# Performance work log

Measured on AMD Instinct MI355X. Metric: run time of the kernel, lower is better.

The kernel has to match this reference:

```python
import jax, jax.numpy as jnp
import numpy as np

N, E, E2 = 50000, 100000, 100000
NODE_IN, H, EDGE_IN, EDGE_H = 64, 32, 16, 128
STEPS = 3
ALPHA = 0.5
BETA = 1.0 / STEPS  # forward overwrites self.beta with 1/num_steps
EPS = 1e-5


def setup_inputs() -> dict:
    key = jax.random.key(0)
    ks = jax.random.split(key, 16)
    p = lambda k, shape, s=0.05: (jax.random.normal(k, shape, jnp.float32) * s)
    return {
        "n_feat": jax.random.normal(ks[0], (N, NODE_IN), jnp.float32),
        "e_feat": jax.random.normal(ks[1], (E, EDGE_IN), jnp.float32),
        "src": jax.random.randint(ks[2], (E,), 0, N, jnp.int32),
        "dst": jax.random.randint(ks[3], (E,), 0, N, jnp.int32),
        "src_list": jax.random.randint(ks[4], (E2,), 0, N, jnp.int32),
        "dst_list": jax.random.randint(ks[5], (E2,), 0, N, jnp.int32),
        "lin0_w": p(ks[6], (H, NODE_IN)), "lin0_b": jnp.zeros((H,), jnp.float32),
        "en1_w": p(ks[7], (EDGE_H, EDGE_IN)), "en1_b": jnp.zeros((EDGE_H,), jnp.float32),
        "en2_w": p(ks[8], (H * H, EDGE_H)), "en2_b": jnp.zeros((H * H,), jnp.float32),
        "conv_bias": jnp.zeros((H,), jnp.float32),
        "lin1_w": p(ks[9], (H, H)), "lin1_b": jnp.zeros((H,), jnp.float32),
        "bn_gamma": jnp.ones((H,), jnp.float32), "bn_beta": jnp.zeros((H,), jnp.float32),
        "ylin_w": p(ks[10], (3, H)), "ylin_b": jnp.zeros((3,), jnp.float32),
        "ylin2_w": p(ks[11], (1, H)), "ylin2_b": jnp.zeros((1,), jnp.float32),
    }


def reference(n_feat, e_feat, src, dst, src_list, dst_list,
              lin0_w, lin0_b, en1_w, en1_b, en2_w, en2_b, conv_bias,
              lin1_w, lin1_b, bn_gamma, bn_beta, ylin_w, ylin_b, ylin2_w, ylin2_b):
    n = n_feat.shape[0]
    out = jax.nn.relu(n_feat @ lin0_w.T + lin0_b)
    h0 = out
    # Edge-conditioned weights (eval mode: dropouts are identity, so the
    # edge MLP output is identical every step -> compute once).
    We = (jax.nn.relu(e_feat @ en1_w.T + en1_b) @ en2_w.T + en2_b).reshape(-1, H, H)  # (E,H,H)
    for _ in range(STEPS):
        msg = jnp.einsum('eh,eho->eo', out[src], We)                 # per-edge matvec
        agg = jax.ops.segment_sum(msg, dst, num_segments=n)          # sum aggregator
        conv = agg + out + conv_bias                                 # identity residual + bias
        temp = ALPHA * conv + (1.0 - ALPHA) * h0
        out = jax.nn.relu(BETA * (temp @ lin1_w.T + lin1_b) + (1.0 - BETA) * temp)
    # BatchNorm1d with batch statistics (training-mode stats, biased var)
    mu = out.mean(axis=0)
    var = ((out - mu) ** 2).mean(axis=0)
    y_bn = (out - mu) / jnp.sqrt(var + EPS) * bn_gamma + bn_beta
    y_sigmoid = jax.nn.sigmoid(y_bn @ ylin_w.T + ylin_b)                              # (N,3)
    edge_hop_out = jax.nn.sigmoid((y_bn[src_list] * y_bn[dst_list]) @ ylin2_w.T + ylin2_b)  # (E2,1)
    return (y_sigmoid, edge_hop_out)
```

## Files before the change

kernel.cpp:

```cpp
#include <hip/hip_runtime.h>
#include <hip/hip_bf16.h>
#include <math.h>

#define HH 32
#define NODE_IN 64
#define EDGE_IN 16
#define EDGE_H 128
#define M_TILE 256

typedef __attribute__((ext_vector_type(8))) short bf16x8;
typedef __attribute__((ext_vector_type(4))) float f32x4;

__device__ inline unsigned short f2bf(float f) {
    union { float f; unsigned int u; } v; v.f = f;
    unsigned int r = v.u + 0x7fff + ((v.u >> 16) & 1);
    return (unsigned short)(r >> 16);
}

__device__ inline void gload_lds16(const void* g, void* lds) {
    __builtin_amdgcn_global_load_lds(
        (const __attribute__((address_space(1))) void*)g,
        (__attribute__((address_space(3))) void*)lds, 16, 0, 0);
}

__global__ void k_prep_w2(const float* __restrict__ en2_w, unsigned short* __restrict__ W2s) {
    int i = blockIdx.x * 256 + threadIdx.x;
    int r = i >> 7, q = i & 127;
    int p = q >> 3, sub = q & 7;
    int c = p ^ (r & 15);
    W2s[i] = f2bf(en2_w[r * EDGE_H + c * 8 + sub]);
}

__global__ void __launch_bounds__(256, 4)
k_prep_r(const float* __restrict__ e_feat, const float* __restrict__ en1_w,
         const float* __restrict__ en1_b, unsigned short* __restrict__ Rb,
         int E, int E_pad) {
    int t = threadIdx.x, wave = t >> 6, l = t & 63;
    int lo = l & 15, lq = l >> 4;
    int ebase = blockIdx.x * 256 + wave * 64;

    bf16x8 bfrag[8];
    #pragma unroll
    for (int nt = 0; nt < 8; ++nt) {
        unsigned short br[8] = {0, 0, 0, 0, 0, 0, 0, 0};
        if (lq < 2) {
            const float* wr = en1_w + (nt * 16 + lo) * EDGE_IN + lq * 8;
            #pragma unroll
            for (int z = 0; z < 8; ++z) br[z] = f2bf(wr[z]);
        }
        bfrag[nt] = *(const bf16x8*)br;
    }
    float b1v[8];
    #pragma unroll
    for (int nt = 0; nt < 8; ++nt) b1v[nt] = en1_b[nt * 16 + lo];

    #pragma unroll
    for (int m = 0; m < 4; ++m) {
        int ea = ebase + m * 16 + lo;
        unsigned short ar[8] = {0, 0, 0, 0, 0, 0, 0, 0};
        if (lq < 2 && ea < E) {
            const float* er = e_feat + (size_t)ea * EDGE_IN + lq * 8;
            float4 v0 = ((const float4*)er)[0];
            float4 v1 = ((const float4*)er)[1];
            ar[0] = f2bf(v0.x); ar[1] = f2bf(v0.y); ar[2] = f2bf(v0.z); ar[3] = f2bf(v0.w);
            ar[4] = f2bf(v1.x); ar[5] = f2bf(v1.y); ar[6] = f2bf(v1.z); ar[7] = f2bf(v1.w);
        }
        bf16x8 af = *(const bf16x8*)ar;

        int erow = ebase + m * 16 + lq * 4;
        #pragma unroll
        for (int nt = 0; nt < 8; ++nt) {
            f32x4 acc = (f32x4){b1v[nt], b1v[nt], b1v[nt], b1v[nt]};
            acc = __builtin_amdgcn_mfma_f32_16x16x32_bf16(af, bfrag[nt], acc, 0, 0, 0);
            #pragma unroll
            for (int r = 0; r < 4; ++r)
                Rb[(size_t)(erow + r) * EDGE_H + nt * 16 + lo] = f2bf(fmaxf(acc[r], 0.f));
        }
    }
}

__global__ void k_lin0(const float* __restrict__ nf, const float* __restrict__ w,
                       const float* __restrict__ b, float* __restrict__ out,
                       float* __restrict__ h0, int n) {
    __shared__ float nf_s[8][NODE_IN];
    __shared__ float w_s[HH][NODE_IN + 1];
    int t = threadIdx.x;
    for (int i = t; i < HH * NODE_IN; i += 256) w_s[i / NODE_IN][i % NODE_IN] = w[i];
    int n0 = blockIdx.x * 8;
    for (int i = t; i < 8 * NODE_IN; i += 256) {
        int nl = i / NODE_IN, k = i % NODE_IN;
        int nn = n0 + nl;
        nf_s[nl][k] = (nn < n) ? nf[(size_t)nn * NODE_IN + k] : 0.f;
    }
    __syncthreads();
    int nl = t >> 5, h = t & 31;
    int nn = n0 + nl;
    if (nn < n) {
        float acc = b[h];
        #pragma unroll
        for (int k = 0; k < NODE_IN; ++k) acc += nf_s[nl][k] * w_s[h][k];
        acc = fmaxf(acc, 0.f);
        out[(size_t)nn * HH + h] = acc;
        h0[(size_t)nn * HH + h] = acc;
    }
}

__global__ void k_zero_int(int* __restrict__ p, int n) {
    int i = blockIdx.x * 256 + threadIdx.x;
    if (i < n) p[i] = 0;
}
__global__ void k_hist(const int* __restrict__ dst, int* __restrict__ deg, int E) {
    int e = blockIdx.x * 256 + threadIdx.x;
    if (e < E) atomicAdd(&deg[dst[e]], 1);
}
__global__ void k_scan1(const int* __restrict__ deg, int* __restrict__ offtmp,
                        int* __restrict__ bsum, int n) {
    __shared__ int sh[256];
    int tid = threadIdx.x;
    int i = blockIdx.x * 256 + tid;
    int v = (i < n) ? deg[i] : 0;
    sh[tid] = v;
    __syncthreads();
    for (int d = 1; d < 256; d <<= 1) {
        int add = (tid >= d) ? sh[tid - d] : 0;
        __syncthreads();
        sh[tid] += add;
        __syncthreads();
    }
    if (i < n) offtmp[i] = sh[tid] - v;
    if (tid == 255) bsum[blockIdx.x] = sh[255];
}
__global__ void k_scan2(int* __restrict__ bsum, int nb) {
    __shared__ int sh[256];
    int tid = threadIdx.x;
    int v = (tid < nb) ? bsum[tid] : 0;
    sh[tid] = v;
    __syncthreads();
    for (int d = 1; d < 256; d <<= 1) {
        int add = (tid >= d) ? sh[tid - d] : 0;
        __syncthreads();
        sh[tid] += add;
        __syncthreads();
    }
    if (tid < nb) bsum[tid] = sh[tid] - v;
}
__global__ void k_scan3(const int* __restrict__ offtmp, const int* __restrict__ bsum,
                        int* __restrict__ offsets, int* __restrict__ cursor, int n, int E) {
    int i = blockIdx.x * 256 + threadIdx.x;
    if (i < n) { offsets[i] = offtmp[i] + bsum[i >> 8]; cursor[i] = 0; }
    if (i == n) offsets[n] = E;
}
__global__ void k_scatter_pos(const int* __restrict__ dst, const int* __restrict__ offsets,
                              int* __restrict__ cursor, int* __restrict__ pos, int E) {
    int e = blockIdx.x * 256 + threadIdx.x;
    if (e < E) pos[e] = offsets[dst[e]] + atomicAdd(&cursor[dst[e]], 1);
}

__global__ void __launch_bounds__(256, 2)
k_edge_mfma5(const unsigned short* __restrict__ Rb, const unsigned short* __restrict__ W2s,
             const float* __restrict__ b2, const float* __restrict__ cur,
             const int* __restrict__ src, const int* __restrict__ pos,
             float* __restrict__ outp, int E) {
    __shared__ unsigned short w2buf[4][32 * EDGE_H];
    __shared__ float x_t[HH][M_TILE];
    __shared__ float b2_s[HH * HH];
    int t = threadIdx.x, wave = t >> 6, l = t & 63;
    int lo = l & 15, lq = l >> 4;
    int e0 = blockIdx.x * M_TILE;

    for (int i = t; i < HH * HH; i += 256) b2_s[i] = b2[i];

    for (int i = t; i < M_TILE * 8; i += 256) {
        int el = i >> 3, c = i & 7;
        int e = e0 + el;
        float4 v = make_float4(0.f, 0.f, 0.f, 0.f);
        if (e < E) v = ((const float4*)(cur + (size_t)src[e] * HH))[c];
        x_t[c * 4 + 0][el] = v.x; x_t[c * 4 + 1][el] = v.y;
        x_t[c * 4 + 2][el] = v.z; x_t[c * 4 + 3][el] = v.w;
    }

    bf16x8 afrag[4][4];
    #pragma unroll
    for (int m = 0; m < 4; ++m)
        #pragma unroll
        for (int ks = 0; ks < 4; ++ks)
            afrag[m][ks] = *(const bf16x8*)(Rb + (size_t)(e0 + wave * 64 + m * 16 + lo) * EDGE_H + ks * 32 + lq * 8);

    #pragma unroll
    for (int s = 0; s < 3; ++s) {
        gload_lds16(W2s + (size_t)s * 4096 + t * 8,        &w2buf[s][t * 8]);
        gload_lds16(W2s + (size_t)s * 4096 + 2048 + t * 8, &w2buf[s][2048 + t * 8]);
    }

    asm volatile("s_waitcnt lgkmcnt(0)" ::: "memory");

    float macc[4][2][4];
    #pragma unroll
    for (int m = 0; m < 4; ++m)
        #pragma unroll
        for (int nn = 0; nn < 2; ++nn)
            #pragma unroll
            for (int r = 0; r < 4; ++r) macc[m][nn][r] = 0.f;

    #pragma unroll 4
    for (int h = 0; h < HH; ++h) {
        if (h < 30)       asm volatile("s_waitcnt vmcnt(4)" ::: "memory");
        else if (h == 30) asm volatile("s_waitcnt vmcnt(2)" ::: "memory");
        else              asm volatile("s_waitcnt vmcnt(0)" ::: "memory");
        __builtin_amdgcn_s_barrier();
        if (h + 3 < HH) {
            gload_lds16(W2s + (size_t)(h + 3) * 4096 + t * 8,        &w2buf[(h + 3) & 3][t * 8]);
            gload_lds16(W2s + (size_t)(h + 3) * 4096 + 2048 + t * 8, &w2buf[(h + 3) & 3][2048 + t * 8]);
        }

        const unsigned short* wb = w2buf[h & 3];
        bf16x8 bfrag[2][4];
        #pragma unroll
        for (int nn = 0; nn < 2; ++nn)
            #pragma unroll
            for (int ks = 0; ks < 4; ++ks)
                bfrag[nn][ks] = *(const bf16x8*)&wb[(nn * 16 + lo) * EDGE_H + (((ks * 4 + lq) ^ lo) * 8)];

        #pragma unroll
        for (int m = 0; m < 4; ++m) {
            f32x4 acc[2];
            #pragma unroll
            for (int nn = 0; nn < 2; ++nn) {
                float bb = b2_s[h * HH + nn * 16 + lo];
                acc[nn] = (f32x4){bb, bb, bb, bb};
            }
            #pragma unroll
            for (int ks = 0; ks < 4; ++ks)
                #pragma unroll
                for (int nn = 0; nn < 2; ++nn)
                    acc[nn] = __builtin_amdgcn_mfma_f32_16x16x32_bf16(
                        afrag[m][ks], bfrag[nn][ks], acc[nn], 0, 0, 0);

            const float4 xv = *(const float4*)&x_t[h][wave * 64 + m * 16 + lq * 4];
            #pragma unroll
            for (int nn = 0; nn < 2; ++nn) {
                macc[m][nn][0] += xv.x * acc[nn][0];
                macc[m][nn][1] += xv.y * acc[nn][1];
                macc[m][nn][2] += xv.z * acc[nn][2];
                macc[m][nn][3] += xv.w * acc[nn][3];
            }
        }
    }

    #pragma unroll
    for (int m = 0; m < 4; ++m) {
        int ebase = e0 + wave * 64 + m * 16 + lq * 4;
        const int4 p4 = *(const int4*)&pos[ebase];
        int pr[4] = { p4.x, p4.y, p4.z, p4.w };
        #pragma unroll
        for (int r = 0; r < 4; ++r) {
            if (ebase + r < E) {
                outp[(size_t)pr[r] * HH + lo]      = macc[m][0][r];
                outp[(size_t)pr[r] * HH + 16 + lo] = macc[m][1][r];
            }
        }
    }
}

__global__ void k_node_update(const float* __restrict__ msg_sorted, const int* __restrict__ offsets,
                              const float* __restrict__ cur, const float* __restrict__ h0,
                              const float* __restrict__ conv_bias,
                              const float* __restrict__ lin1_w, const float* __restrict__ lin1_b,
                              float* __restrict__ nxt, int n) {
    __shared__ float t_s[8][HH + 1];
    __shared__ float w_s[HH][HH + 1];
    int t = threadIdx.x;
    for (int i = t; i < HH * HH; i += 256) w_s[i >> 5][i & 31] = lin1_w[i];
    int nl = t >> 5, h = t & 31;
    int nn = blockIdx.x * 8 + nl;
    float tv = 0.f;
    if (nn < n) {
        int s0 = offsets[nn], s1 = offsets[nn + 1];
        float s = 0.f;
        for (int i = s0; i < s1; ++i) s += msg_sorted[(size_t)i * HH + h];
        size_t idx = (size_t)nn * HH + h;
        float conv = s + cur[idx] + conv_bias[h];
        tv = 0.5f * conv + 0.5f * h0[idx];
    }
    t_s[nl][h] = tv;
    __syncthreads();
    if (nn < n) {
        const float BETA = 1.0f / 3.0f;
        float d = lin1_b[h];
        #pragma unroll
        for (int k = 0; k < HH; ++k) d += t_s[nl][k] * w_s[h][k];
        float v = BETA * d + (1.0f - BETA) * tv;
        nxt[(size_t)nn * HH + h] = fmaxf(v, 0.f);
    }
}

__global__ void k_bn_stats(const float* __restrict__ out, float* __restrict__ stats, int n) {
    int t = threadIdx.x;
    int h = t & 31, rg = t >> 5;
    float s = 0.f, s2 = 0.f;
    for (int nn = blockIdx.x * 8 + rg; nn < n; nn += gridDim.x * 8) {
        float v = out[(size_t)nn * HH + h];
        s += v; s2 += v * v;
    }
    __shared__ float sh[256], sh2[256];
    sh[t] = s; sh2[t] = s2;
    __syncthreads();
    if (rg == 0) {
        #pragma unroll
        for (int g = 1; g < 8; ++g) { s += sh[g * 32 + h]; s2 += sh2[g * 32 + h]; }
        atomicAdd(&stats[h], s);
        atomicAdd(&stats[32 + h], s2);
    }
}

__global__ void k_node_out(const float* __restrict__ out, const float* __restrict__ stats,
                           const float* __restrict__ gamma, const float* __restrict__ beta,
                           const float* __restrict__ ylin_w, const float* __restrict__ ylin_b,
                           float* __restrict__ y_bn, float* __restrict__ y_sig, int n) {
    int nn = blockIdx.x * blockDim.x + threadIdx.x;
    if (nn >= n) return;
    float inv_n = 1.f / (float)n;
    float yb[HH];
    #pragma unroll
    for (int h = 0; h < HH; ++h) {
        float mu = stats[h] * inv_n;
        float var = stats[32 + h] * inv_n - mu * mu;
        float v = out[(size_t)nn * HH + h];
        yb[h] = (v - mu) * rsqrtf(var + 1e-5f) * gamma[h] + beta[h];
    }
    #pragma unroll
    for (int h = 0; h < HH; ++h) y_bn[(size_t)nn * HH + h] = yb[h];
    #pragma unroll
    for (int c = 0; c < 3; ++c) {
        float d = ylin_b[c];
        #pragma unroll
        for (int h = 0; h < HH; ++h) d += yb[h] * ylin_w[c * HH + h];
        y_sig[(size_t)nn * 3 + c] = 1.f / (1.f + expf(-d));
    }
}

__global__ void k_edge_hop(const float* __restrict__ y_bn, const int* __restrict__ sl,
                           const int* __restrict__ dl, const float* __restrict__ w,
                           const float* __restrict__ b, float* __restrict__ outp, int e2) {
    int e = blockIdx.x * blockDim.x + threadIdx.x;
    if (e >= e2) return;
    const float4* a = (const float4*)(y_bn + (size_t)sl[e] * HH);
    const float4* c = (const float4*)(y_bn + (size_t)dl[e] * HH);
    float d = b[0];
    #pragma unroll
    for (int q = 0; q < 8; ++q) {
        float4 av = a[q], cv = c[q];
        float4 wv = ((const float4*)w)[q];
        d += av.x * cv.x * wv.x + av.y * cv.y * wv.y + av.z * cv.z * wv.z + av.w * cv.w * wv.w;
    }
    outp[e] = 1.f / (1.f + expf(-d));
}

extern "C" void kernel_launch(void* const* d_in, const int* in_sizes, int n_in,
                              void* d_out, int out_size, void* d_ws, size_t ws_size,
                              hipStream_t stream) {
    const float* n_feat   = (const float*)d_in[0];
    const float* e_feat   = (const float*)d_in[1];
    const int*   src      = (const int*)d_in[2];
    const int*   dst      = (const int*)d_in[3];
    const int*   src_list = (const int*)d_in[4];
    const int*   dst_list = (const int*)d_in[5];
    const float* lin0_w   = (const float*)d_in[6];
    const float* lin0_b   = (const float*)d_in[7];
    const float* en1_w    = (const float*)d_in[8];
    const float* en1_b    = (const float*)d_in[9];
    const float* en2_w    = (const float*)d_in[10];
    const float* en2_b    = (const float*)d_in[11];
    const float* conv_bias= (const float*)d_in[12];
    const float* lin1_w   = (const float*)d_in[13];
    const float* lin1_b   = (const float*)d_in[14];
    const float* bn_gamma = (const float*)d_in[15];
    const float* bn_beta  = (const float*)d_in[16];
    const float* ylin_w   = (const float*)d_in[17];
    const float* ylin_b   = (const float*)d_in[18];
    const float* ylin2_w  = (const float*)d_in[19];
    const float* ylin2_b  = (const float*)d_in[20];

    int n  = in_sizes[0] / NODE_IN;
    int E  = in_sizes[1] / EDGE_IN;
    int e2 = in_sizes[4];
    int E_pad = (E + M_TILE - 1) & ~(M_TILE - 1);

    float* ws    = (float*)d_ws;
    size_t nh    = (size_t)n * HH;
    float* out_a = ws;
    float* out_b = out_a + nh;
    float* h0    = out_b + nh;
    float* y_bn  = h0 + nh;
    float* stats = y_bn + nh;
    float* msg_sorted = stats + 64;
    unsigned short* W2s = (unsigned short*)(msg_sorted + (size_t)E_pad * HH);
    unsigned short* Rb  = W2s + 1024 * EDGE_H;
    int* ibase   = (int*)(Rb + (size_t)E_pad * EDGE_H);
    int* deg     = ibase;
    int* offtmp  = deg + n;
    int* bsum    = offtmp + n;
    int* offsets = bsum + 256;
    int* cursor  = offsets + n + 1;
    int* pos     = cursor + n;

    int nb = (n + 255) / 256;

    k_prep_w2<<<(1024 * EDGE_H) / 256, 256, 0, stream>>>(en2_w, W2s);
    k_prep_r<<<E_pad / 256, 256, 0, stream>>>(e_feat, en1_w, en1_b, Rb, E, E_pad);
    k_lin0<<<(n + 7) / 8, 256, 0, stream>>>(n_feat, lin0_w, lin0_b, out_a, h0, n);

    k_zero_int<<<nb, 256, 0, stream>>>(deg, n);
    k_hist<<<(E + 255) / 256, 256, 0, stream>>>(dst, deg, E);
    k_scan1<<<nb, 256, 0, stream>>>(deg, offtmp, bsum, n);
    k_scan2<<<1, 256, 0, stream>>>(bsum, nb);
    k_scan3<<<(n + 256) / 256, 256, 0, stream>>>(offtmp, bsum, offsets, cursor, n, E);
    k_scatter_pos<<<(E + 255) / 256, 256, 0, stream>>>(dst, offsets, cursor, pos, E);

    const float* cur = out_a;
    float* nxt = out_b;
    for (int s = 0; s < 3; ++s) {
        k_edge_mfma5<<<E_pad / M_TILE, 256, 0, stream>>>(
            Rb, W2s, en2_b, cur, src, pos, msg_sorted, E);
        k_node_update<<<(n + 7) / 8, 256, 0, stream>>>(
            msg_sorted, offsets, cur, h0, conv_bias, lin1_w, lin1_b, nxt, n);
        float* t = (float*)cur; cur = nxt; nxt = t;
    }

    hipMemsetAsync(stats, 0, 64 * sizeof(float), stream);
    k_bn_stats<<<256, 256, 0, stream>>>(cur, stats, n);

    float* y_sig = (float*)d_out;
    float* e_out = y_sig + (size_t)n * 3;
    k_node_out<<<(n + 255) / 256, 256, 0, stream>>>(
        cur, stats, bn_gamma, bn_beta, ylin_w, ylin_b, y_bn, y_sig, n);
    k_edge_hop<<<(e2 + 255) / 256, 256, 0, stream>>>(
        y_bn, src_list, dst_list, ylin2_w, ylin2_b, e_out, e2);
}
```

Measured before the change: 274.6 us.

## Replace CSR sort-based aggregation with atomic scatter-add and halve edge tile

Drops the degree histogram, scan and position-scatter kernels and the sorted message buffer. The edge kernel now atomically adds each message directly into a zeroed per-node aggregate, so the node update reads one value instead of looping over its CSR segment. The edge tile shrinks from 256 to 128 edges, with three blocks per CU and s_setprio around the MFMA section, to raise occupancy. The cost is float atomic contention, a memset on every step, and summation that is no longer deterministic.

```diff
diff --git a/kernel.cpp b/kernel.cpp
--- a/kernel.cpp
+++ b/kernel.cpp
@@ -6,7 +6,8 @@
 #define NODE_IN 64
 #define EDGE_IN 16
 #define EDGE_H 128
-#define M_TILE 256
+#define M_TILE 128
+#define E_PAD_UNIT 256
 
 typedef __attribute__((ext_vector_type(8))) short bf16x8;
 typedef __attribute__((ext_vector_type(4))) float f32x4;
@@ -105,64 +106,13 @@
     }
 }
 
-__global__ void k_zero_int(int* __restrict__ p, int n) {
-    int i = blockIdx.x * 256 + threadIdx.x;
-    if (i < n) p[i] = 0;
-}
-__global__ void k_hist(const int* __restrict__ dst, int* __restrict__ deg, int E) {
-    int e = blockIdx.x * 256 + threadIdx.x;
-    if (e < E) atomicAdd(&deg[dst[e]], 1);
-}
-__global__ void k_scan1(const int* __restrict__ deg, int* __restrict__ offtmp,
-                        int* __restrict__ bsum, int n) {
-    __shared__ int sh[256];
-    int tid = threadIdx.x;
-    int i = blockIdx.x * 256 + tid;
-    int v = (i < n) ? deg[i] : 0;
-    sh[tid] = v;
-    __syncthreads();
-    for (int d = 1; d < 256; d <<= 1) {
-        int add = (tid >= d) ? sh[tid - d] : 0;
-        __syncthreads();
-        sh[tid] += add;
-        __syncthreads();
-    }
-    if (i < n) offtmp[i] = sh[tid] - v;
-    if (tid == 255) bsum[blockIdx.x] = sh[255];
-}
-__global__ void k_scan2(int* __restrict__ bsum, int nb) {
-    __shared__ int sh[256];
-    int tid = threadIdx.x;
-    int v = (tid < nb) ? bsum[tid] : 0;
-    sh[tid] = v;
-    __syncthreads();
-    for (int d = 1; d < 256; d <<= 1) {
-        int add = (tid >= d) ? sh[tid - d] : 0;
-        __syncthreads();
-        sh[tid] += add;
-        __syncthreads();
-    }
-    if (tid < nb) bsum[tid] = sh[tid] - v;
-}
-__global__ void k_scan3(const int* __restrict__ offtmp, const int* __restrict__ bsum,
-                        int* __restrict__ offsets, int* __restrict__ cursor, int n, int E) {
-    int i = blockIdx.x * 256 + threadIdx.x;
-    if (i < n) { offsets[i] = offtmp[i] + bsum[i >> 8]; cursor[i] = 0; }
-    if (i == n) offsets[n] = E;
-}
-__global__ void k_scatter_pos(const int* __restrict__ dst, const int* __restrict__ offsets,
-                              int* __restrict__ cursor, int* __restrict__ pos, int E) {
-    int e = blockIdx.x * 256 + threadIdx.x;
-    if (e < E) pos[e] = offsets[dst[e]] + atomicAdd(&cursor[dst[e]], 1);
-}
-
-__global__ void __launch_bounds__(256, 2)
-k_edge_mfma5(const unsigned short* __restrict__ Rb, const unsigned short* __restrict__ W2s,
+__global__ void __launch_bounds__(256, 3)
+k_edge_mfma6(const unsigned short* __restrict__ Rb, const unsigned short* __restrict__ W2s,
              const float* __restrict__ b2, const float* __restrict__ cur,
-             const int* __restrict__ src, const int* __restrict__ pos,
-             float* __restrict__ outp, int E) {
+             const int* __restrict__ src, const int* __restrict__ dst,
+             float* __restrict__ agg, int E) {
     __shared__ unsigned short w2buf[4][32 * EDGE_H];
-    __shared__ float x_t[HH][M_TILE];
+    __shared__ float x_t[HH][M_TILE + 4];
     __shared__ float b2_s[HH * HH];
     int t = threadIdx.x, wave = t >> 6, l = t & 63;
     int lo = l & 15, lq = l >> 4;
@@ -179,12 +129,12 @@
         x_t[c * 4 + 2][el] = v.z; x_t[c * 4 + 3][el] = v.w;
     }
 
-    bf16x8 afrag[4][4];
-    #pragma unroll
-    for (int m = 0; m < 4; ++m)
+    bf16x8 afrag[2][4];
+    #pragma unroll
+    for (int m = 0; m < 2; ++m)
         #pragma unroll
         for (int ks = 0; ks < 4; ++ks)
-            afrag[m][ks] = *(const bf16x8*)(Rb + (size_t)(e0 + wave * 64 + m * 16 + lo) * EDGE_H + ks * 32 + lq * 8);
+            afrag[m][ks] = *(const bf16x8*)(Rb + (size_t)(e0 + wave * 32 + m * 16 + lo) * EDGE_H + ks * 32 + lq * 8);
 
     #pragma unroll
     for (int s = 0; s < 3; ++s) {
@@ -194,9 +144,9 @@
 
     asm volatile("s_waitcnt lgkmcnt(0)" ::: "memory");
 
-    float macc[4][2][4];
-    #pragma unroll
-    for (int m = 0; m < 4; ++m)
+    float macc[2][2][4];
+    #pragma unroll
+    for (int m = 0; m < 2; ++m)
         #pragma unroll
         for (int nn = 0; nn < 2; ++nn)
             #pragma unroll
@@ -221,8 +171,9 @@
             for (int ks = 0; ks < 4; ++ks)
                 bfrag[nn][ks] = *(const bf16x8*)&wb[(nn * 16 + lo) * EDGE_H + (((ks * 4 + lq) ^ lo) * 8)];
 
-        #pragma unroll
-        for (int m = 0; m < 4; ++m) {
+        __builtin_amdgcn_s_setprio(1);
+        #pragma unroll
+        for (int m = 0; m < 2; ++m) {
             f32x4 acc[2];
             #pragma unroll
             for (int nn = 0; nn < 2; ++nn) {
@@ -236,7 +187,7 @@
                     acc[nn] = __builtin_amdgcn_mfma_f32_16x16x32_bf16(
                         afrag[m][ks], bfrag[nn][ks], acc[nn], 0, 0, 0);
 
-            const float4 xv = *(const float4*)&x_t[h][wave * 64 + m * 16 + lq * 4];
+            const float4 xv = *(const float4*)&x_t[h][wave * 32 + m * 16 + lq * 4];
             #pragma unroll
             for (int nn = 0; nn < 2; ++nn) {
                 macc[m][nn][0] += xv.x * acc[nn][0];
@@ -245,24 +196,25 @@
                 macc[m][nn][3] += xv.w * acc[nn][3];
             }
         }
-    }
-
-    #pragma unroll
-    for (int m = 0; m < 4; ++m) {
-        int ebase = e0 + wave * 64 + m * 16 + lq * 4;
-        const int4 p4 = *(const int4*)&pos[ebase];
-        int pr[4] = { p4.x, p4.y, p4.z, p4.w };
+        __builtin_amdgcn_s_setprio(0);
+    }
+
+    #pragma unroll
+    for (int m = 0; m < 2; ++m) {
+        int ebase = e0 + wave * 32 + m * 16 + lq * 4;
         #pragma unroll
         for (int r = 0; r < 4; ++r) {
-            if (ebase + r < E) {
-                outp[(size_t)pr[r] * HH + lo]      = macc[m][0][r];
-                outp[(size_t)pr[r] * HH + 16 + lo] = macc[m][1][r];
+            int e = ebase + r;
+            if (e < E) {
+                int d = dst[e];
+                atomicAdd(&agg[(size_t)d * HH + lo],      macc[m][0][r]);
+                atomicAdd(&agg[(size_t)d * HH + 16 + lo], macc[m][1][r]);
             }
         }
     }
 }
 
-__global__ void k_node_update(const float* __restrict__ msg_sorted, const int* __restrict__ offsets,
+__global__ void k_node_update(const float* __restrict__ agg,
                               const float* __restrict__ cur, const float* __restrict__ h0,
                               const float* __restrict__ conv_bias,
                               const float* __restrict__ lin1_w, const float* __restrict__ lin1_b,
@@ -275,11 +227,8 @@
     int nn = blockIdx.x * 8 + nl;
     float tv = 0.f;
     if (nn < n) {
-        int s0 = offsets[nn], s1 = offsets[nn + 1];
-        float s = 0.f;
-        for (int i = s0; i < s1; ++i) s += msg_sorted[(size_t)i * HH + h];
         size_t idx = (size_t)nn * HH + h;
-        float conv = s + cur[idx] + conv_bias[h];
+        float conv = agg[idx] + cur[idx] + conv_bias[h];
         tv = 0.5f * conv + 0.5f * h0[idx];
     }
     t_s[nl][h] = tv;
@@ -384,7 +333,7 @@
     int n  = in_sizes[0] / NODE_IN;
     int E  = in_sizes[1] / EDGE_IN;
     int e2 = in_sizes[4];
-    int E_pad = (E + M_TILE - 1) & ~(M_TILE - 1);
+    int E_pad = (E + E_PAD_UNIT - 1) & ~(E_PAD_UNIT - 1);
 
     float* ws    = (float*)d_ws;
     size_t nh    = (size_t)n * HH;
@@ -392,38 +341,23 @@
     float* out_b = out_a + nh;
     float* h0    = out_b + nh;
     float* y_bn  = h0 + nh;
-    float* stats = y_bn + nh;
-    float* msg_sorted = stats + 64;
-    unsigned short* W2s = (unsigned short*)(msg_sorted + (size_t)E_pad * HH);
+    float* agg   = y_bn + nh;
+    float* stats = agg + nh;
+    unsigned short* W2s = (unsigned short*)(stats + 64);
     unsigned short* Rb  = W2s + 1024 * EDGE_H;
-    int* ibase   = (int*)(Rb + (size_t)E_pad * EDGE_H);
-    int* deg     = ibase;
-    int* offtmp  = deg + n;
-    int* bsum    = offtmp + n;
-    int* offsets = bsum + 256;
-    int* cursor  = offsets + n + 1;
-    int* pos     = cursor + n;
-
-    int nb = (n + 255) / 256;
 
     k_prep_w2<<<(1024 * EDGE_H) / 256, 256, 0, stream>>>(en2_w, W2s);
     k_prep_r<<<E_pad / 256, 256, 0, stream>>>(e_feat, en1_w, en1_b, Rb, E, E_pad);
     k_lin0<<<(n + 7) / 8, 256, 0, stream>>>(n_feat, lin0_w, lin0_b, out_a, h0, n);
 
-    k_zero_int<<<nb, 256, 0, stream>>>(deg, n);
-    k_hist<<<(E + 255) / 256, 256, 0, stream>>>(dst, deg, E);
-    k_scan1<<<nb, 256, 0, stream>>>(deg, offtmp, bsum, n);
-    k_scan2<<<1, 256, 0, stream>>>(bsum, nb);
-    k_scan3<<<(n + 256) / 256, 256, 0, stream>>>(offtmp, bsum, offsets, cursor, n, E);
-    k_scatter_pos<<<(E + 255) / 256, 256, 0, stream>>>(dst, offsets, cursor, pos, E);
-
     const float* cur = out_a;
     float* nxt = out_b;
     for (int s = 0; s < 3; ++s) {
-        k_edge_mfma5<<<E_pad / M_TILE, 256, 0, stream>>>(
-            Rb, W2s, en2_b, cur, src, pos, msg_sorted, E);
+        hipMemsetAsync(agg, 0, nh * sizeof(float), stream);
+        k_edge_mfma6<<<E_pad / M_TILE, 256, 0, stream>>>(
+            Rb, W2s, en2_b, cur, src, dst, agg, E);
         k_node_update<<<(n + 7) / 8, 256, 0, stream>>>(
-            msg_sorted, offsets, cur, h0, conv_bias, lin1_w, lin1_b, nxt, n);
+            agg, cur, h0, conv_bias, lin1_w, lin1_b, nxt, n);
         float* t = (float*)cur; cur = nxt; nxt = t;
     }
 
```

Result: no change. 277.0 us, median of 4 (+0.9%).

## Make edge kernel persistent with W2 held in registers per wave

Applied to the files above, without the earlier changes.

Replaces the per-block streaming of the whole W2 matrix through LDS with a persistent kernel of 256 blocks of 8 waves. Each wave keeps a fixed 4-row slice of W2 in registers and loops over 64-edge tiles. The gathered source features are double-buffered in LDS, and per-wave partial sums are reduced through LDS before the sorted-message write. This aims to remove the repeated W2 global-to-LDS traffic and barriers per block, at the cost of heavy register pressure, re-reading Rb fragments in every wave, and extra LDS reduction and syncs per tile.

```diff
diff --git a/kernel.cpp b/kernel.cpp
--- a/kernel.cpp
+++ b/kernel.cpp
@@ -6,7 +6,8 @@
 #define NODE_IN 64
 #define EDGE_IN 16
 #define EDGE_H 128
-#define M_TILE 256
+#define ET8 64
+#define E_PAD_UNIT 256
 
 typedef __attribute__((ext_vector_type(8))) short bf16x8;
 typedef __attribute__((ext_vector_type(4))) float f32x4;
@@ -17,18 +18,9 @@
     return (unsigned short)(r >> 16);
 }
 
-__device__ inline void gload_lds16(const void* g, void* lds) {
-    __builtin_amdgcn_global_load_lds(
-        (const __attribute__((address_space(1))) void*)g,
-        (__attribute__((address_space(3))) void*)lds, 16, 0, 0);
-}
-
-__global__ void k_prep_w2(const float* __restrict__ en2_w, unsigned short* __restrict__ W2s) {
+__global__ void k_prep_w2(const float* __restrict__ en2_w, unsigned short* __restrict__ W2b) {
     int i = blockIdx.x * 256 + threadIdx.x;
-    int r = i >> 7, q = i & 127;
-    int p = q >> 3, sub = q & 7;
-    int c = p ^ (r & 15);
-    W2s[i] = f2bf(en2_w[r * EDGE_H + c * 8 + sub]);
+    W2b[i] = f2bf(en2_w[i]);
 }
 
 __global__ void __launch_bounds__(256, 4)
@@ -156,109 +148,133 @@
     if (e < E) pos[e] = offsets[dst[e]] + atomicAdd(&cursor[dst[e]], 1);
 }
 
-__global__ void __launch_bounds__(256, 2)
-k_edge_mfma5(const unsigned short* __restrict__ Rb, const unsigned short* __restrict__ W2s,
+__global__ void __launch_bounds__(512, 2)
+k_edge_mfma8(const unsigned short* __restrict__ Rb, const unsigned short* __restrict__ W2b,
              const float* __restrict__ b2, const float* __restrict__ cur,
              const int* __restrict__ src, const int* __restrict__ pos,
-             float* __restrict__ outp, int E) {
-    __shared__ unsigned short w2buf[4][32 * EDGE_H];
-    __shared__ float x_t[HH][M_TILE];
-    __shared__ float b2_s[HH * HH];
+             float* __restrict__ outp, int E, int tiles) {
+    __shared__ float x_t[2][HH][ET8 + 4];
+    __shared__ float slots[4][ET8 * 33];
     int t = threadIdx.x, wave = t >> 6, l = t & 63;
     int lo = l & 15, lq = l >> 4;
-    int e0 = blockIdx.x * M_TILE;
-
-    for (int i = t; i < HH * HH; i += 256) b2_s[i] = b2[i];
-
-    for (int i = t; i < M_TILE * 8; i += 256) {
-        int el = i >> 3, c = i & 7;
-        int e = e0 + el;
-        float4 v = make_float4(0.f, 0.f, 0.f, 0.f);
-        if (e < E) v = ((const float4*)(cur + (size_t)src[e] * HH))[c];
-        x_t[c * 4 + 0][el] = v.x; x_t[c * 4 + 1][el] = v.y;
-        x_t[c * 4 + 2][el] = v.z; x_t[c * 4 + 3][el] = v.w;
-    }
-
-    bf16x8 afrag[4][4];
-    #pragma unroll
-    for (int m = 0; m < 4; ++m)
-        #pragma unroll
-        for (int ks = 0; ks < 4; ++ks)
-            afrag[m][ks] = *(const bf16x8*)(Rb + (size_t)(e0 + wave * 64 + m * 16 + lo) * EDGE_H + ks * 32 + lq * 8);
-
-    #pragma unroll
-    for (int s = 0; s < 3; ++s) {
-        gload_lds16(W2s + (size_t)s * 4096 + t * 8,        &w2buf[s][t * 8]);
-        gload_lds16(W2s + (size_t)s * 4096 + 2048 + t * 8, &w2buf[s][2048 + t * 8]);
-    }
-
-    asm volatile("s_waitcnt lgkmcnt(0)" ::: "memory");
-
-    float macc[4][2][4];
-    #pragma unroll
-    for (int m = 0; m < 4; ++m)
-        #pragma unroll
-        for (int nn = 0; nn < 2; ++nn)
-            #pragma unroll
-            for (int r = 0; r < 4; ++r) macc[m][nn][r] = 0.f;
-
-    #pragma unroll 4
-    for (int h = 0; h < HH; ++h) {
-        if (h < 30)       asm volatile("s_waitcnt vmcnt(4)" ::: "memory");
-        else if (h == 30) asm volatile("s_waitcnt vmcnt(2)" ::: "memory");
-        else              asm volatile("s_waitcnt vmcnt(0)" ::: "memory");
-        __builtin_amdgcn_s_barrier();
-        if (h + 3 < HH) {
-            gload_lds16(W2s + (size_t)(h + 3) * 4096 + t * 8,        &w2buf[(h + 3) & 3][t * 8]);
-            gload_lds16(W2s + (size_t)(h + 3) * 4096 + 2048 + t * 8, &w2buf[(h + 3) & 3][2048 + t * 8]);
-        }
-
-        const unsigned short* wb = w2buf[h & 3];
-        bf16x8 bfrag[2][4];
-        #pragma unroll
-        for (int nn = 0; nn < 2; ++nn)
+
+    bf16x8 bfrag[4][2][4];
+    float b2v[4][2];
+    #pragma unroll
+    for (int hh = 0; hh < 4; ++hh) {
+        int h = wave * 4 + hh;
+        #pragma unroll
+        for (int nn = 0; nn < 2; ++nn) {
+            b2v[hh][nn] = b2[h * HH + nn * 16 + lo];
             #pragma unroll
             for (int ks = 0; ks < 4; ++ks)
-                bfrag[nn][ks] = *(const bf16x8*)&wb[(nn * 16 + lo) * EDGE_H + (((ks * 4 + lq) ^ lo) * 8)];
-
-        #pragma unroll
-        for (int m = 0; m < 4; ++m) {
-            f32x4 acc[2];
-            #pragma unroll
-            for (int nn = 0; nn < 2; ++nn) {
-                float bb = b2_s[h * HH + nn * 16 + lo];
-                acc[nn] = (f32x4){bb, bb, bb, bb};
+                bfrag[hh][nn][ks] = *(const bf16x8*)(W2b + (size_t)(h * HH + nn * 16 + lo) * EDGE_H + ks * 32 + lq * 8);
+        }
+    }
+
+    {
+        int e0 = blockIdx.x * ET8;
+        for (int i = t; i < ET8 * 8; i += 512) {
+            int el = i >> 3, c = i & 7;
+            int e = e0 + el;
+            float4 v = make_float4(0.f, 0.f, 0.f, 0.f);
+            if (e < E) v = ((const float4*)(cur + (size_t)src[e] * HH))[c];
+            x_t[0][c * 4 + 0][el] = v.x; x_t[0][c * 4 + 1][el] = v.y;
+            x_t[0][c * 4 + 2][el] = v.z; x_t[0][c * 4 + 3][el] = v.w;
+        }
+    }
+    __syncthreads();
+
+    int it = 0;
+    for (int tile = blockIdx.x; tile < tiles; tile += gridDim.x, ++it) {
+        int cb = it & 1;
+        int e0 = tile * ET8;
+
+        int ntile = tile + gridDim.x;
+        if (ntile < tiles) {
+            int ne0 = ntile * ET8;
+            for (int i = t; i < ET8 * 8; i += 512) {
+                int el = i >> 3, c = i & 7;
+                int e = ne0 + el;
+                float4 v = make_float4(0.f, 0.f, 0.f, 0.f);
+                if (e < E) v = ((const float4*)(cur + (size_t)src[e] * HH))[c];
+                x_t[cb ^ 1][c * 4 + 0][el] = v.x; x_t[cb ^ 1][c * 4 + 1][el] = v.y;
+                x_t[cb ^ 1][c * 4 + 2][el] = v.z; x_t[cb ^ 1][c * 4 + 3][el] = v.w;
             }
-            #pragma unroll
-            for (int ks = 0; ks < 4; ++ks)
+        }
+
+        float macc[4][2][4];
+        #pragma unroll
+        for (int m = 0; m < 4; ++m)
+            #pragma unroll
+            for (int nn = 0; nn < 2; ++nn)
+                #pragma unroll
+                for (int r = 0; r < 4; ++r) macc[m][nn][r] = 0.f;
+
+        #pragma unroll
+        for (int mh = 0; mh < 2; ++mh) {
+            bf16x8 af[2][4];
+            #pragma unroll
+            for (int mi = 0; mi < 2; ++mi)
+                #pragma unroll
+                for (int ks = 0; ks < 4; ++ks)
+                    af[mi][ks] = *(const bf16x8*)(Rb + (size_t)(e0 + (mh * 2 + mi) * 16 + lo) * EDGE_H + ks * 32 + lq * 8);
+
+            #pragma unroll
+            for (int hh = 0; hh < 4; ++hh) {
+                int h = wave * 4 + hh;
+                #pragma unroll
+                for (int mi = 0; mi < 2; ++mi) {
+                    f32x4 acc[2];
+                    acc[0] = (f32x4){b2v[hh][0], b2v[hh][0], b2v[hh][0], b2v[hh][0]};
+                    acc[1] = (f32x4){b2v[hh][1], b2v[hh][1], b2v[hh][1], b2v[hh][1]};
+                    #pragma unroll
+                    for (int ks = 0; ks < 4; ++ks)
+                        #pragma unroll
+                        for (int nn = 0; nn < 2; ++nn)
+                            acc[nn] = __builtin_amdgcn_mfma_f32_16x16x32_bf16(
+                                af[mi][ks], bfrag[hh][nn][ks], acc[nn], 0, 0, 0);
+                    const float4 xv = *(const float4*)&x_t[cb][h][(mh * 2 + mi) * 16 + lq * 4];
+                    #pragma unroll
+                    for (int nn = 0; nn < 2; ++nn) {
+                        macc[mh * 2 + mi][nn][0] += xv.x * acc[nn][0];
+                        macc[mh * 2 + mi][nn][1] += xv.y * acc[nn][1];
+                        macc[mh * 2 + mi][nn][2] += xv.z * acc[nn][2];
+                        macc[mh * 2 + mi][nn][3] += xv.w * acc[nn][3];
+                    }
+                }
+            }
+        }
+
+        if (wave < 4) {
+            #pragma unroll
+            for (int m = 0; m < 4; ++m)
                 #pragma unroll
                 for (int nn = 0; nn < 2; ++nn)
-                    acc[nn] = __builtin_amdgcn_mfma_f32_16x16x32_bf16(
-                        afrag[m][ks], bfrag[nn][ks], acc[nn], 0, 0, 0);
-
-            const float4 xv = *(const float4*)&x_t[h][wave * 64 + m * 16 + lq * 4];
-            #pragma unroll
-            for (int nn = 0; nn < 2; ++nn) {
-                macc[m][nn][0] += xv.x * acc[nn][0];
-                macc[m][nn][1] += xv.y * acc[nn][1];
-                macc[m][nn][2] += xv.z * acc[nn][2];
-                macc[m][nn][3] += xv.w * acc[nn][3];
-            }
-        }
-    }
-
-    #pragma unroll
-    for (int m = 0; m < 4; ++m) {
-        int ebase = e0 + wave * 64 + m * 16 + lq * 4;
-        const int4 p4 = *(const int4*)&pos[ebase];
-        int pr[4] = { p4.x, p4.y, p4.z, p4.w };
-        #pragma unroll
-        for (int r = 0; r < 4; ++r) {
-            if (ebase + r < E) {
-                outp[(size_t)pr[r] * HH + lo]      = macc[m][0][r];
-                outp[(size_t)pr[r] * HH + 16 + lo] = macc[m][1][r];
-            }
-        }
+                    #pragma unroll
+                    for (int r = 0; r < 4; ++r)
+                        slots[wave][(m * 16 + lq * 4 + r) * 33 + nn * 16 + lo] = macc[m][nn][r];
+        }
+        __syncthreads();
+        if (wave >= 4) {
+            #pragma unroll
+            for (int m = 0; m < 4; ++m)
+                #pragma unroll
+                for (int nn = 0; nn < 2; ++nn)
+                    #pragma unroll
+                    for (int r = 0; r < 4; ++r)
+                        slots[wave - 4][(m * 16 + lq * 4 + r) * 33 + nn * 16 + lo] += macc[m][nn][r];
+        }
+        __syncthreads();
+
+        for (int i = t; i < ET8 * HH; i += 512) {
+            int row = i >> 5, col = i & 31;
+            float s = slots[0][row * 33 + col] + slots[1][row * 33 + col]
+                    + slots[2][row * 33 + col] + slots[3][row * 33 + col];
+            int e = e0 + row;
+            if (e < E) outp[(size_t)pos[e] * HH + col] = s;
+        }
+        __syncthreads();
     }
 }
 
@@ -384,7 +400,8 @@
     int n  = in_sizes[0] / NODE_IN;
     int E  = in_sizes[1] / EDGE_IN;
     int e2 = in_sizes[4];
-    int E_pad = (E + M_TILE - 1) & ~(M_TILE - 1);
+    int E_pad = (E + E_PAD_UNIT - 1) & ~(E_PAD_UNIT - 1);
+    int tiles = E_pad / ET8;
 
     float* ws    = (float*)d_ws;
     size_t nh    = (size_t)n * HH;
@@ -394,8 +411,8 @@
     float* y_bn  = h0 + nh;
     float* stats = y_bn + nh;
     float* msg_sorted = stats + 64;
-    unsigned short* W2s = (unsigned short*)(msg_sorted + (size_t)E_pad * HH);
-    unsigned short* Rb  = W2s + 1024 * EDGE_H;
+    unsigned short* W2b = (unsigned short*)(msg_sorted + (size_t)E_pad * HH);
+    unsigned short* Rb  = W2b + 1024 * EDGE_H;
     int* ibase   = (int*)(Rb + (size_t)E_pad * EDGE_H);
     int* deg     = ibase;
     int* offtmp  = deg + n;
@@ -406,7 +423,7 @@
 
     int nb = (n + 255) / 256;
 
-    k_prep_w2<<<(1024 * EDGE_H) / 256, 256, 0, stream>>>(en2_w, W2s);
+    k_prep_w2<<<(1024 * EDGE_H) / 256, 256, 0, stream>>>(en2_w, W2b);
     k_prep_r<<<E_pad / 256, 256, 0, stream>>>(e_feat, en1_w, en1_b, Rb, E, E_pad);
     k_lin0<<<(n + 7) / 8, 256, 0, stream>>>(n_feat, lin0_w, lin0_b, out_a, h0, n);
 
@@ -420,8 +437,8 @@
     const float* cur = out_a;
     float* nxt = out_b;
     for (int s = 0; s < 3; ++s) {
-        k_edge_mfma5<<<E_pad / M_TILE, 256, 0, stream>>>(
-            Rb, W2s, en2_b, cur, src, pos, msg_sorted, E);
+        k_edge_mfma8<<<256, 512, 0, stream>>>(
+            Rb, W2b, en2_b, cur, src, pos, msg_sorted, E, tiles);
         k_node_update<<<(n + 7) / 8, 256, 0, stream>>>(
             msg_sorted, offsets, cur, h0, conv_bias, lin1_w, lin1_b, nxt, n);
         float* t = (float*)cur; cur = nxt; nxt = t;
```

Result: slower. 302.2 us (+10.0%).
